# Optimization experiments

Measured on AMD Instinct MI355X. Metric: run time of the kernel, lower is better.

## Reference

```python
import jax, jax.numpy as jnp
import numpy as np

B = 2097152
IND = 10
DIM = 32
L = 4
M = DIM // 2 + 1  # 17 rfft bins
EPS = 1e-5


def setup_inputs() -> dict:
    key = jax.random.key(0)
    ks = jax.random.split(key, 16)
    scale = 1.0 / (DIM * DIM)
    inp = {
        'x': jax.random.normal(ks[0], (B, IND), dtype=jnp.float32),
        # stem / head Linear weights stored as [in, out] (x @ W + b)
        'stem_w': jax.random.normal(ks[1], (IND, DIM), jnp.float32) * (1.0 / np.sqrt(IND)),
        'stem_b': jnp.zeros((DIM,), jnp.float32),
        # Fourier weights: torch.rand complex -> real & imag ~ U[0,1), scaled
        'fno_wr': scale * jax.random.uniform(ks[2], (L, M, M), jnp.float32),
        'fno_wi': scale * jax.random.uniform(ks[3], (L, M, M), jnp.float32),
        # ResidualBlock params, stacked over layers
        'bn1_g': jnp.ones((L, DIM), jnp.float32),
        'bn1_b': jnp.zeros((L, DIM), jnp.float32),
        'lin1_w': jax.random.normal(ks[4], (L, DIM, DIM), jnp.float32) * (1.0 / np.sqrt(DIM)),
        'lin1_b': jnp.zeros((L, DIM), jnp.float32),
        'bn2_g': jnp.ones((L, DIM), jnp.float32),
        'bn2_b': jnp.zeros((L, DIM), jnp.float32),
        'lin2_w': jax.random.normal(ks[5], (L, DIM, DIM), jnp.float32) * (1.0 / np.sqrt(DIM)),
        'lin2_b': jnp.zeros((L, DIM), jnp.float32),
        'head_w': jax.random.normal(ks[6], (DIM, IND), jnp.float32) * (1.0 / np.sqrt(DIM)),
        'head_b': jnp.zeros((IND,), jnp.float32),
    }
    return inp


def _bn(h, g, b):
    # BatchNorm1d in training mode: biased batch stats over the batch dim
    mu = jnp.mean(h, axis=0)
    var = jnp.mean(jnp.square(h - mu), axis=0)
    return (h - mu) * jax.lax.rsqrt(var + EPS) * g + b


def reference(x, stem_w, stem_b, fno_wr, fno_wi, bn1_g, bn1_b, lin1_w, lin1_b,
              bn2_g, bn2_b, lin2_w, lin2_b, head_w, head_b):
    h = x @ stem_w + stem_b  # [B, DIM]
    n_layers = fno_wr.shape[0]
    for i in range(n_layers):
        # FourierBlock: rfft -> complex channel mix -> irfft (bias=False)
        w = fno_wr[i] + 1j * fno_wi[i]  # [M, M] complex
        hf = jnp.fft.rfft(h, axis=-1)  # [B, M] complex
        x1 = jnp.fft.irfft(hf @ w, n=DIM, axis=-1)  # [B, DIM]
        # ResidualBlock: BN -> SiLU -> Linear -> BN -> SiLU -> Linear, + identity skip
        r = jax.nn.silu(_bn(h, bn1_g[i], bn1_b[i])) @ lin1_w[i] + lin1_b[i]
        r = jax.nn.silu(_bn(r, bn2_g[i], bn2_b[i])) @ lin2_w[i] + lin2_b[i]
        x2 = r + h
        h = jax.nn.silu(x1 + x2)
    return h @ head_w + head_b  # [B, IND]
```

## Files before the change

### kernel.cpp

```cpp
#include <hip/hip_runtime.h>
#include <math.h>

#define BATCH   2097152
#define NTILES  (BATCH / 16)
#define GRID    2048
#define BLOCK   256
#define WAVES   (GRID * (BLOCK / 64))
#define NREP    16
#define NSETS   8

typedef __attribute__((ext_vector_type(8))) short short8;
typedef __attribute__((ext_vector_type(4))) float f32x4;
typedef unsigned short ushort_t;

__device__ __forceinline__ int chan_of(int s) { return (s >> 1) + ((s & 1) << 4); }

__device__ __forceinline__ float silu_f(float x) {
    return x * __builtin_amdgcn_rcpf(1.0f + __expf(-x));
}
__device__ __forceinline__ unsigned cvt_pk_bf16(float lo, float hi) {
    unsigned r;
    asm("v_cvt_pk_bf16_f32 %0, %1, %2" : "=v"(r) : "v"(lo), "v"(hi));
    return r;
}
__device__ __forceinline__ unsigned short f2bf(float f) {
    union { float f; unsigned u; } v; v.f = f;
    unsigned r = v.u + 0x7fffu + ((v.u >> 16) & 1u);
    return (unsigned short)(r >> 16);
}
__device__ __forceinline__ float bf2f(unsigned short b) {
    union { unsigned u; float f; } v; v.u = ((unsigned)b) << 16;
    return v.f;
}
__device__ __forceinline__ short8 pack8(const float* f) {
    union { short8 s; unsigned u[4]; } r;
    #pragma unroll
    for (int i = 0; i < 4; ++i) r.u[i] = cvt_pk_bf16(f[2 * i], f[2 * i + 1]);
    return r.s;
}
__device__ __forceinline__ f32x4 mfma16(short8 a, short8 b, f32x4 c) {
    return __builtin_amdgcn_mfma_f32_16x16x32_bf16(a, b, c, 0, 0, 0);
}
__device__ __forceinline__ short8 wfrag(const float* W, int ldN, int K, int lane, int half, int N) {
    short8 r;
    const int n = (lane & 15) + 16 * half;
    const int k0 = (lane >> 4) * 8;
    #pragma unroll
    for (int j = 0; j < 8; ++j) {
        const int ck = chan_of(k0 + j);
        const float v = (ck < K && n < N) ? W[ck * ldN + n] : 0.f;
        ((unsigned short*)&r)[j] = f2bf(v);
    }
    return r;
}
__device__ __forceinline__ void bn_coef(const double* sIn, const float* g, const float* b,
                                        int c, float* A, float* C) {
    double s = 0, q = 0;
    #pragma unroll
    for (int r = 0; r < NREP; ++r) { s += sIn[r * 64 + c]; q += sIn[r * 64 + 32 + c]; }
    const double inv = 1.0 / (double)BATCH;
    const double mu = s * inv, var = q * inv - mu * mu;
    const float a = (float)(1.0 / sqrt(var + 1e-5)) * g[c];
    *A = a; *C = b[c] - (float)mu * a;
}
__device__ __forceinline__ void stats_reduce_c(float sS0, float sQ0, float sS1, float sQ1,
                                               float (*sRed)[64], double* sOut, int tid) {
    const int lane = tid & 63, wid = tid >> 6;
    sS0 += __shfl_down(sS0, 32); sS0 += __shfl_down(sS0, 16);
    sQ0 += __shfl_down(sQ0, 32); sQ0 += __shfl_down(sQ0, 16);
    sS1 += __shfl_down(sS1, 32); sS1 += __shfl_down(sS1, 16);
    sQ1 += __shfl_down(sQ1, 32); sQ1 += __shfl_down(sQ1, 16);
    if (lane < 16) {
        sRed[wid][lane] = sS0; sRed[wid][16 + lane] = sS1;
        sRed[wid][32 + lane] = sQ0; sRed[wid][48 + lane] = sQ1;
    }
    __syncthreads();
    if (tid < 64) {
        const float tot = sRed[0][tid] + sRed[1][tid] + sRed[2][tid] + sRed[3][tid];
        atomicAdd(sOut + tid, (double)tot);
    }
}
__device__ __forceinline__ void stats_reduce_r(float* sLo, float* sQLo, float* sHi, float* sQHi,
                                               float (*sRed)[64], double* sOut, int tid) {
    const int lane = tid & 63, wid = tid >> 6, q = lane >> 4;
    #pragma unroll
    for (int r = 0; r < 4; ++r) {
        #pragma unroll
        for (int off = 8; off; off >>= 1) {
            sLo[r]  += __shfl_down(sLo[r],  off);
            sQLo[r] += __shfl_down(sQLo[r], off);
            sHi[r]  += __shfl_down(sHi[r],  off);
            sQHi[r] += __shfl_down(sQHi[r], off);
        }
    }
    if ((lane & 15) == 0) {
        #pragma unroll
        for (int r = 0; r < 4; ++r) {
            sRed[wid][q * 4 + r]      = sLo[r];
            sRed[wid][16 + q * 4 + r] = sHi[r];
            sRed[wid][32 + q * 4 + r] = sQLo[r];
            sRed[wid][48 + q * 4 + r] = sQHi[r];
        }
    }
    __syncthreads();
    if (tid < 64) {
        const float tot = sRed[0][tid] + sRed[1][tid] + sRed[2][tid] + sRed[3][tid];
        atomicAdd(sOut + tid, (double)tot);
    }
}

__global__ void setup_f_kernel(const float* __restrict__ wr, const float* __restrict__ wi,
                               float* __restrict__ Fp)
{
    __shared__ double cs[32], sn[32];
    const int l = blockIdx.x, tid = threadIdx.x;
    if (tid < 32) {
        double a = (2.0 * 3.14159265358979323846 / 32.0) * (double)tid;
        cs[tid] = cos(a); sn[tid] = sin(a);
    }
    __syncthreads();
    const float* wrl = wr + l * 289;
    const float* wil = wi + l * 289;
    for (int p = tid; p < 1024; p += BLOCK) {
        const int d = p >> 5, j = p & 31;
        double acc = 0.0;
        for (int m = 0; m < 17; ++m) {
            double yr = 0.0, yi = 0.0;
            for (int k = 0; k < 17; ++k) {
                const double c = cs[(k * d) & 31], s = sn[(k * d) & 31];
                const double a = (double)wrl[k * 17 + m], b = (double)wil[k * 17 + m];
                yr += c * a + s * b;
                yi += c * b - s * a;
            }
            const double alpha = (m == 0 || m == 16) ? 1.0 : 2.0;
            acc += alpha * (cs[(j * m) & 31] * yr - sn[(j * m) & 31] * yi);
        }
        const double F = acc * (1.0 / 32.0);
        Fp[l * 1024 + d * 32 + j] = (float)(F + ((d == j) ? 1.0 : 0.0));
    }
}

__global__ __launch_bounds__(BLOCK) void stem_kernel(
    const float* __restrict__ x, const float* __restrict__ sw, const float* __restrict__ sb,
    ushort_t* __restrict__ h, double* __restrict__ sOut)
{
    __shared__ float sRed[4][64];
    const int tid = threadIdx.x, lane = tid & 63, wid = tid >> 6;
    const int m = lane & 15, q = lane >> 4;
    const short8 B0 = wfrag(sw, 32, 10, lane, 0, 32);
    const short8 B1 = wfrag(sw, 32, 10, lane, 1, 32);
    float sblo[4], sbhi[4];
    #pragma unroll
    for (int r = 0; r < 4; ++r) { sblo[r] = sb[q * 4 + r]; sbhi[r] = sb[16 + q * 4 + r]; }
    float sLo[4] = {0,0,0,0}, sQLo[4] = {0,0,0,0}, sHi[4] = {0,0,0,0}, sQHi[4] = {0,0,0,0};
    for (int t = blockIdx.x * (BLOCK / 64) + wid; t < NTILES; t += WAVES) {
        const size_t rb = (size_t)t * 16;
        float c4[4];
        #pragma unroll
        for (int i2 = 0; i2 < 2; ++i2) {
            const int k = q * 4 + 2 * i2;
            if (k + 1 < 10) {
                const float2 v = *(const float2*)(x + (rb + m) * 10 + k);
                c4[2 * i2] = v.x; c4[2 * i2 + 1] = v.y;
            } else { c4[2 * i2] = 0.f; c4[2 * i2 + 1] = 0.f; }
        }
        float xv[8];
        #pragma unroll
        for (int j = 0; j < 8; ++j) xv[j] = (j & 1) ? 0.f : c4[j >> 1];
        const short8 xa = pack8(xv);
        f32x4 a0 = {sblo[0], sblo[1], sblo[2], sblo[3]};
        f32x4 a1 = {sbhi[0], sbhi[1], sbhi[2], sbhi[3]};
        a0 = mfma16(B0, xa, a0);
        a1 = mfma16(B1, xa, a1);
        #pragma unroll
        for (int r = 0; r < 4; ++r) {
            sLo[r] += a0[r]; sQLo[r] += a0[r] * a0[r];
            sHi[r] += a1[r]; sQHi[r] += a1[r] * a1[r];
            const unsigned w = cvt_pk_bf16(a0[r], a1[r]);
            *(unsigned*)(h + (rb + m) * 32 + (size_t)(q * 4 + r) * 2) = w;
        }
    }
    stats_reduce_r(sLo, sQLo, sHi, sQHi, sRed, sOut + (size_t)(blockIdx.x & (NREP - 1)) * 64, tid);
}

__global__ __launch_bounds__(BLOCK) void p1_kernel(
    const ushort_t* __restrict__ h_in, const double* __restrict__ sIn, double* __restrict__ sOut,
    const float* __restrict__ g1, const float* __restrict__ b1,
    const float* __restrict__ w1, const float* __restrict__ lb1)
{
    __shared__ float cA[32], cC[32];
    __shared__ float sRed[4][64];
    const int tid = threadIdx.x, lane = tid & 63, wid = tid >> 6;
    if (tid < 32) bn_coef(sIn, g1, b1, tid, &cA[tid], &cC[tid]);
    __syncthreads();
    const int m = lane & 15, q = lane >> 4;
    float a1k[8], c1k[8];
    #pragma unroll
    for (int j = 0; j < 8; ++j) {
        const int c = chan_of(q * 8 + j);
        a1k[j] = cA[c]; c1k[j] = cC[c];
    }
    const short8 W10 = wfrag(w1, 32, 32, lane, 0, 32);
    const short8 W11 = wfrag(w1, 32, 32, lane, 1, 32);
    const float lbc0 = lb1[m], lbc1 = lb1[m + 16];
    float sS0 = 0, sQ0 = 0, sS1 = 0, sQ1 = 0;
    for (int t = blockIdx.x * (BLOCK / 64) + wid; t < NTILES; t += WAVES) {
        const size_t rb = (size_t)t * 16;
        const short8 ha = *(const short8*)(h_in + (rb + m) * 32 + q * 8);
        float tf[8];
        #pragma unroll
        for (int j = 0; j < 8; ++j)
            tf[j] = silu_f(a1k[j] * bf2f(((const unsigned short*)&ha)[j]) + c1k[j]);
        const short8 ta = pack8(tf);
        f32x4 r0 = {lbc0, lbc0, lbc0, lbc0}, r1 = {lbc1, lbc1, lbc1, lbc1};
        r0 = mfma16(ta, W10, r0);
        r1 = mfma16(ta, W11, r1);
        #pragma unroll
        for (int r = 0; r < 4; ++r) {
            sS0 += r0[r]; sQ0 += r0[r] * r0[r];
            sS1 += r1[r]; sQ1 += r1[r] * r1[r];
        }
    }
    stats_reduce_c(sS0, sQ0, sS1, sQ1, sRed, sOut + (size_t)(blockIdx.x & (NREP - 1)) * 64, tid);
}

template<bool LAST>
__global__ __launch_bounds__(BLOCK) void p2_kernel(
    const ushort_t* __restrict__ h_in, ushort_t* __restrict__ h_out, float* __restrict__ out,
    const double* __restrict__ sIn1, const double* __restrict__ sIn2, double* __restrict__ sOut,
    const float* __restrict__ g1, const float* __restrict__ b1,
    const float* __restrict__ w1, const float* __restrict__ lb1,
    const float* __restrict__ g2, const float* __restrict__ b2,
    const float* __restrict__ w2, const float* __restrict__ lb2,
    const float* __restrict__ Fp, const float* __restrict__ hw, const float* __restrict__ hb)
{
    __shared__ float cA1[32], cC1[32], cA2[32], cD2[32];
    __shared__ float sRed[4][64];
    const int tid = threadIdx.x, lane = tid & 63, wid = tid >> 6;
    if (tid < 32) {
        bn_coef(sIn1, g1, b1, tid, &cA1[tid], &cC1[tid]);
    } else if (tid < 64) {
        const int c = tid - 32;
        float A, C;
        bn_coef(sIn2, g2, b2, c, &A, &C);
        cA2[c] = A; cD2[c] = C + A * lb1[c];
    }
    __syncthreads();
    const int m = lane & 15, q = lane >> 4;
    float a1k[8], c1k[8];
    #pragma unroll
    for (int j = 0; j < 8; ++j) {
        const int c = chan_of(q * 8 + j);
        a1k[j] = cA1[c]; c1k[j] = cC1[c];
    }
    float a2lo[4], d2lo[4], a2hi[4], d2hi[4], blo[4], bhi[4], hbl[4];
    #pragma unroll
    for (int r = 0; r < 4; ++r) {
        const int c = q * 4 + r;
        a2lo[r] = cA2[c];      d2lo[r] = cD2[c];
        a2hi[r] = cA2[c + 16]; d2hi[r] = cD2[c + 16];
        blo[r] = lb2[c];       bhi[r] = lb2[c + 16];
        hbl[r] = (LAST && c < 10) ? hb[c] : 0.f;
    }
    const short8 W10 = wfrag(w1, 32, 32, lane, 0, 32);
    const short8 W11 = wfrag(w1, 32, 32, lane, 1, 32);
    const short8 W20 = wfrag(w2, 32, 32, lane, 0, 32);
    const short8 W21 = wfrag(w2, 32, 32, lane, 1, 32);
    const short8 F0  = wfrag(Fp, 32, 32, lane, 0, 32);
    const short8 F1  = wfrag(Fp, 32, 32, lane, 1, 32);
    short8 HW = {};
    if (LAST) HW = wfrag(hw, 10, 32, lane, 0, 10);
    float sLo[4] = {0,0,0,0}, sQLo[4] = {0,0,0,0}, sHi[4] = {0,0,0,0}, sQHi[4] = {0,0,0,0};

    for (int t = blockIdx.x * (BLOCK / 64) + wid; t < NTILES; t += WAVES) {
        const size_t rb = (size_t)t * 16;
        const short8 ha = *(const short8*)(h_in + (rb + m) * 32 + q * 8);
        float tf[8];
        #pragma unroll
        for (int j = 0; j < 8; ++j)
            tf[j] = silu_f(a1k[j] * bf2f(((const unsigned short*)&ha)[j]) + c1k[j]);
        const short8 ta = pack8(tf);
        const f32x4 z = {0.f, 0.f, 0.f, 0.f};
        f32x4 r0 = mfma16(W10, ta, z);
        f32x4 r1 = mfma16(W11, ta, z);
        float ulo[4], uhi[4];
        #pragma unroll
        for (int r = 0; r < 4; ++r) {
            ulo[r] = silu_f(a2lo[r] * r0[r] + d2lo[r]);
            uhi[r] = silu_f(a2hi[r] * r1[r] + d2hi[r]);
        }
        union { short8 s; unsigned u[4]; } uau;
        #pragma unroll
        for (int i = 0; i < 4; ++i) uau.u[i] = cvt_pk_bf16(ulo[i], uhi[i]);
        const short8 ua = uau.s;
        f32x4 c0 = {blo[0], blo[1], blo[2], blo[3]};
        f32x4 c1 = {bhi[0], bhi[1], bhi[2], bhi[3]};
        c0 = mfma16(F0, ha, c0);  c1 = mfma16(F1, ha, c1);
        c0 = mfma16(W20, ua, c0); c1 = mfma16(W21, ua, c1);
        float hnlo[4], hnhi[4];
        #pragma unroll
        for (int r = 0; r < 4; ++r) { hnlo[r] = silu_f(c0[r]); hnhi[r] = silu_f(c1[r]); }
        if (!LAST) {
            #pragma unroll
            for (int r = 0; r < 4; ++r) {
                sLo[r] += hnlo[r]; sQLo[r] += hnlo[r] * hnlo[r];
                sHi[r] += hnhi[r]; sQHi[r] += hnhi[r] * hnhi[r];
                const unsigned w = cvt_pk_bf16(hnlo[r], hnhi[r]);
                *(unsigned*)(h_out + (rb + m) * 32 + (size_t)(q * 4 + r) * 2) = w;
            }
        } else {
            union { short8 s; unsigned u[4]; } hnu;
            #pragma unroll
            for (int i = 0; i < 4; ++i) hnu.u[i] = cvt_pk_bf16(hnlo[i], hnhi[i]);
            f32x4 oc = {hbl[0], hbl[1], hbl[2], hbl[3]};
            oc = mfma16(HW, hnu.s, oc);
            #pragma unroll
            for (int r = 0; r < 4; ++r)
                if (q * 4 + r < 10) out[(rb + m) * 10 + q * 4 + r] = oc[r];
        }
    }
    if (!LAST)
        stats_reduce_r(sLo, sQLo, sHi, sQHi, sRed, sOut + (size_t)(blockIdx.x & (NREP - 1)) * 64, tid);
}

extern "C" void kernel_launch(void* const* d_in, const int* in_sizes, int n_in,
                              void* d_out, int out_size, void* d_ws, size_t ws_size,
                              hipStream_t stream)
{
    const float* x      = (const float*)d_in[0];
    const float* stem_w = (const float*)d_in[1];
    const float* stem_b = (const float*)d_in[2];
    const float* fno_wr = (const float*)d_in[3];
    const float* fno_wi = (const float*)d_in[4];
    const float* bn1_g  = (const float*)d_in[5];
    const float* bn1_b  = (const float*)d_in[6];
    const float* lin1_w = (const float*)d_in[7];
    const float* lin1_b = (const float*)d_in[8];
    const float* bn2_g  = (const float*)d_in[9];
    const float* bn2_b  = (const float*)d_in[10];
    const float* lin2_w = (const float*)d_in[11];
    const float* lin2_b = (const float*)d_in[12];
    const float* head_w = (const float*)d_in[13];
    const float* head_b = (const float*)d_in[14];

    ushort_t* h  = (ushort_t*)d_ws;
    float*    Fp = (float*)((char*)d_ws + (size_t)BATCH * 32 * sizeof(ushort_t));
    double*   st = (double*)((char*)d_ws + (size_t)BATCH * 32 * sizeof(ushort_t) + 16384);

    hipMemsetAsync(st, 0, (size_t)NSETS * NREP * 64 * sizeof(double), stream);
    setup_f_kernel<<<4, BLOCK, 0, stream>>>(fno_wr, fno_wi, Fp);
    stem_kernel<<<GRID, BLOCK, 0, stream>>>(x, stem_w, stem_b, h, st);

    for (int l = 0; l < 4; ++l) {
        double* sH = st + (size_t)(2 * l) * NREP * 64;
        double* sR = st + (size_t)(2 * l + 1) * NREP * 64;
        p1_kernel<<<GRID, BLOCK, 0, stream>>>(
            h, sH, sR,
            bn1_g + l * 32, bn1_b + l * 32, lin1_w + l * 1024, lin1_b + l * 32);
        if (l < 3) {
            double* sN = st + (size_t)(2 * l + 2) * NREP * 64;
            p2_kernel<false><<<GRID, BLOCK, 0, stream>>>(
                h, h, nullptr, sH, sR, sN,
                bn1_g + l * 32, bn1_b + l * 32, lin1_w + l * 1024, lin1_b + l * 32,
                bn2_g + l * 32, bn2_b + l * 32, lin2_w + l * 1024, lin2_b + l * 32,
                Fp + l * 1024, nullptr, nullptr);
        } else {
            p2_kernel<true><<<GRID, BLOCK, 0, stream>>>(
                h, nullptr, (float*)d_out, sH, sR, st,
                bn1_g + l * 32, bn1_b + l * 32, lin1_w + l * 1024, lin1_b + l * 32,
                bn2_g + l * 32, bn2_b + l * 32, lin2_w + l * 1024, lin2_b + l * 32,
                Fp + l * 1024, head_w, head_b);
        }
    }
}
```

Before: 634.1 us.

## Cache BN1+SiLU activations from p1 for reuse in p2; vectorize stores

When the workspace is large enough, p1 writes the bf16 BN1+SiLU activation tile to a second buffer and p2 loads it instead of recomputing the normalization and SiLU. The h stores in stem and p2 are merged into single 16-byte short8 writes, and the head output uses float2 stores. This trades per-element exp/rcp work in p2 for an extra 128 MB write in p1 and read in p2 per layer. On a kernel that is already memory-bound, that extra traffic may cost more than the compute it saves.

```diff
diff --git a/kernel.cpp b/kernel.cpp
--- a/kernel.cpp
+++ b/kernel.cpp
@@ -172,19 +172,22 @@
         f32x4 a1 = {sbhi[0], sbhi[1], sbhi[2], sbhi[3]};
         a0 = mfma16(B0, xa, a0);
         a1 = mfma16(B1, xa, a1);
+        union { short8 s; unsigned u[4]; } hw_;
         #pragma unroll
         for (int r = 0; r < 4; ++r) {
             sLo[r] += a0[r]; sQLo[r] += a0[r] * a0[r];
             sHi[r] += a1[r]; sQHi[r] += a1[r] * a1[r];
-            const unsigned w = cvt_pk_bf16(a0[r], a1[r]);
-            *(unsigned*)(h + (rb + m) * 32 + (size_t)(q * 4 + r) * 2) = w;
-        }
+            hw_.u[r] = cvt_pk_bf16(a0[r], a1[r]);
+        }
+        *(short8*)(h + (rb + m) * 32 + q * 8) = hw_.s;
     }
     stats_reduce_r(sLo, sQLo, sHi, sQHi, sRed, sOut + (size_t)(blockIdx.x & (NREP - 1)) * 64, tid);
 }
 
+template<bool STORE_T>
 __global__ __launch_bounds__(BLOCK) void p1_kernel(
-    const ushort_t* __restrict__ h_in, const double* __restrict__ sIn, double* __restrict__ sOut,
+    const ushort_t* __restrict__ h_in, ushort_t* __restrict__ t_out,
+    const double* __restrict__ sIn, double* __restrict__ sOut,
     const float* __restrict__ g1, const float* __restrict__ b1,
     const float* __restrict__ w1, const float* __restrict__ lb1)
 {
@@ -212,6 +215,8 @@
         for (int j = 0; j < 8; ++j)
             tf[j] = silu_f(a1k[j] * bf2f(((const unsigned short*)&ha)[j]) + c1k[j]);
         const short8 ta = pack8(tf);
+        if (STORE_T)
+            *(short8*)(t_out + (rb + m) * 32 + q * 8) = ta;
         f32x4 r0 = {lbc0, lbc0, lbc0, lbc0}, r1 = {lbc1, lbc1, lbc1, lbc1};
         r0 = mfma16(ta, W10, r0);
         r1 = mfma16(ta, W11, r1);
@@ -224,9 +229,10 @@
     stats_reduce_c(sS0, sQ0, sS1, sQ1, sRed, sOut + (size_t)(blockIdx.x & (NREP - 1)) * 64, tid);
 }
 
-template<bool LAST>
+template<bool LAST, bool TLOAD>
 __global__ __launch_bounds__(BLOCK) void p2_kernel(
-    const ushort_t* __restrict__ h_in, ushort_t* __restrict__ h_out, float* __restrict__ out,
+    const ushort_t* __restrict__ h_in, const ushort_t* __restrict__ t_in,
+    ushort_t* __restrict__ h_out, float* __restrict__ out,
     const double* __restrict__ sIn1, const double* __restrict__ sIn2, double* __restrict__ sOut,
     const float* __restrict__ g1, const float* __restrict__ b1,
     const float* __restrict__ w1, const float* __restrict__ lb1,
@@ -248,10 +254,12 @@
     __syncthreads();
     const int m = lane & 15, q = lane >> 4;
     float a1k[8], c1k[8];
-    #pragma unroll
-    for (int j = 0; j < 8; ++j) {
-        const int c = chan_of(q * 8 + j);
-        a1k[j] = cA1[c]; c1k[j] = cC1[c];
+    if (!TLOAD) {
+        #pragma unroll
+        for (int j = 0; j < 8; ++j) {
+            const int c = chan_of(q * 8 + j);
+            a1k[j] = cA1[c]; c1k[j] = cC1[c];
+        }
     }
     float a2lo[4], d2lo[4], a2hi[4], d2hi[4], blo[4], bhi[4], hbl[4];
     #pragma unroll
@@ -275,11 +283,16 @@
     for (int t = blockIdx.x * (BLOCK / 64) + wid; t < NTILES; t += WAVES) {
         const size_t rb = (size_t)t * 16;
         const short8 ha = *(const short8*)(h_in + (rb + m) * 32 + q * 8);
-        float tf[8];
-        #pragma unroll
-        for (int j = 0; j < 8; ++j)
-            tf[j] = silu_f(a1k[j] * bf2f(((const unsigned short*)&ha)[j]) + c1k[j]);
-        const short8 ta = pack8(tf);
+        short8 ta;
+        if (TLOAD) {
+            ta = *(const short8*)(t_in + (rb + m) * 32 + q * 8);
+        } else {
+            float tf[8];
+            #pragma unroll
+            for (int j = 0; j < 8; ++j)
+                tf[j] = silu_f(a1k[j] * bf2f(((const unsigned short*)&ha)[j]) + c1k[j]);
+            ta = pack8(tf);
+        }
         const f32x4 z = {0.f, 0.f, 0.f, 0.f};
         f32x4 r0 = mfma16(W10, ta, z);
         f32x4 r1 = mfma16(W11, ta, z);
@@ -300,23 +313,28 @@
         float hnlo[4], hnhi[4];
         #pragma unroll
         for (int r = 0; r < 4; ++r) { hnlo[r] = silu_f(c0[r]); hnhi[r] = silu_f(c1[r]); }
+        union { short8 s; unsigned u[4]; } hnu;
+        #pragma unroll
+        for (int r = 0; r < 4; ++r) hnu.u[r] = cvt_pk_bf16(hnlo[r], hnhi[r]);
         if (!LAST) {
             #pragma unroll
             for (int r = 0; r < 4; ++r) {
                 sLo[r] += hnlo[r]; sQLo[r] += hnlo[r] * hnlo[r];
                 sHi[r] += hnhi[r]; sQHi[r] += hnhi[r] * hnhi[r];
-                const unsigned w = cvt_pk_bf16(hnlo[r], hnhi[r]);
-                *(unsigned*)(h_out + (rb + m) * 32 + (size_t)(q * 4 + r) * 2) = w;
             }
+            *(short8*)(h_out + (rb + m) * 32 + q * 8) = hnu.s;
         } else {
-            union { short8 s; unsigned u[4]; } hnu;
-            #pragma unroll
-            for (int i = 0; i < 4; ++i) hnu.u[i] = cvt_pk_bf16(hnlo[i], hnhi[i]);
             f32x4 oc = {hbl[0], hbl[1], hbl[2], hbl[3]};
             oc = mfma16(HW, hnu.s, oc);
-            #pragma unroll
-            for (int r = 0; r < 4; ++r)
-                if (q * 4 + r < 10) out[(rb + m) * 10 + q * 4 + r] = oc[r];
+            float* op = out + (rb + m) * 10 + q * 4;
+            if (q < 2) {
+                float2 v0; v0.x = oc[0]; v0.y = oc[1];
+                float2 v1; v1.x = oc[2]; v1.y = oc[3];
+                *(float2*)op = v0; *(float2*)(op + 2) = v1;
+            } else if (q == 2) {
+                float2 v0; v0.x = oc[0]; v0.y = oc[1];
+                *(float2*)op = v0;
+            }
         }
     }
     if (!LAST)
@@ -343,9 +361,15 @@
     const float* head_w = (const float*)d_in[13];
     const float* head_b = (const float*)d_in[14];
 
+    const size_t HBYTES = (size_t)BATCH * 32 * sizeof(ushort_t);
+    const size_t TAIL   = 16384 + (size_t)NSETS * NREP * 64 * sizeof(double);
+    const bool   big    = ws_size >= 2 * HBYTES + TAIL;
+
     ushort_t* h  = (ushort_t*)d_ws;
-    float*    Fp = (float*)((char*)d_ws + (size_t)BATCH * 32 * sizeof(ushort_t));
-    double*   st = (double*)((char*)d_ws + (size_t)BATCH * 32 * sizeof(ushort_t) + 16384);
+    ushort_t* tw = big ? (ushort_t*)((char*)d_ws + HBYTES) : nullptr;
+    char*     tp = (char*)d_ws + (big ? 2 * HBYTES : HBYTES);
+    float*    Fp = (float*)tp;
+    double*   st = (double*)(tp + 16384);
 
     hipMemsetAsync(st, 0, (size_t)NSETS * NREP * 64 * sizeof(double), stream);
     setup_f_kernel<<<4, BLOCK, 0, stream>>>(fno_wr, fno_wi, Fp);
@@ -354,22 +378,39 @@
     for (int l = 0; l < 4; ++l) {
         double* sH = st + (size_t)(2 * l) * NREP * 64;
         double* sR = st + (size_t)(2 * l + 1) * NREP * 64;
-        p1_kernel<<<GRID, BLOCK, 0, stream>>>(
-            h, sH, sR,
-            bn1_g + l * 32, bn1_b + l * 32, lin1_w + l * 1024, lin1_b + l * 32);
-        if (l < 3) {
-            double* sN = st + (size_t)(2 * l + 2) * NREP * 64;
-            p2_kernel<false><<<GRID, BLOCK, 0, stream>>>(
-                h, h, nullptr, sH, sR, sN,
-                bn1_g + l * 32, bn1_b + l * 32, lin1_w + l * 1024, lin1_b + l * 32,
-                bn2_g + l * 32, bn2_b + l * 32, lin2_w + l * 1024, lin2_b + l * 32,
-                Fp + l * 1024, nullptr, nullptr);
+        double* sN = (l < 3) ? st + (size_t)(2 * l + 2) * NREP * 64 : st;
+        if (big) {
+            p1_kernel<true><<<GRID, BLOCK, 0, stream>>>(
+                h, tw, sH, sR,
+                bn1_g + l * 32, bn1_b + l * 32, lin1_w + l * 1024, lin1_b + l * 32);
+            if (l < 3)
+                p2_kernel<false, true><<<GRID, BLOCK, 0, stream>>>(
+                    h, tw, h, nullptr, sH, sR, sN,
+                    bn1_g + l * 32, bn1_b + l * 32, lin1_w + l * 1024, lin1_b + l * 32,
+                    bn2_g + l * 32, bn2_b + l * 32, lin2_w + l * 1024, lin2_b + l * 32,
+                    Fp + l * 1024, nullptr, nullptr);
+            else
+                p2_kernel<true, true><<<GRID, BLOCK, 0, stream>>>(
+                    h, tw, nullptr, (float*)d_out, sH, sR, st,
+                    bn1_g + l * 32, bn1_b + l * 32, lin1_w + l * 1024, lin1_b + l * 32,
+                    bn2_g + l * 32, bn2_b + l * 32, lin2_w + l * 1024, lin2_b + l * 32,
+                    Fp + l * 1024, head_w, head_b);
         } else {
-            p2_kernel<true><<<GRID, BLOCK, 0, stream>>>(
-                h, nullptr, (float*)d_out, sH, sR, st,
-                bn1_g + l * 32, bn1_b + l * 32, lin1_w + l * 1024, lin1_b + l * 32,
-                bn2_g + l * 32, bn2_b + l * 32, lin2_w + l * 1024, lin2_b + l * 32,
-                Fp + l * 1024, head_w, head_b);
-        }
-    }
-}
+            p1_kernel<false><<<GRID, BLOCK, 0, stream>>>(
+                h, nullptr, sH, sR,
+                bn1_g + l * 32, bn1_b + l * 32, lin1_w + l * 1024, lin1_b + l * 32);
+            if (l < 3)
+                p2_kernel<false, false><<<GRID, BLOCK, 0, stream>>>(
+                    h, nullptr, h, nullptr, sH, sR, sN,
+                    bn1_g + l * 32, bn1_b + l * 32, lin1_w + l * 1024, lin1_b + l * 32,
+                    bn2_g + l * 32, bn2_b + l * 32, lin2_w + l * 1024, lin2_b + l * 32,
+                    Fp + l * 1024, nullptr, nullptr);
+            else
+                p2_kernel<true, false><<<GRID, BLOCK, 0, stream>>>(
+                    h, nullptr, nullptr, (float*)d_out, sH, sR, st,
+                    bn1_g + l * 32, bn1_b + l * 32, lin1_w + l * 1024, lin1_b + l * 32,
+                    bn2_g + l * 32, bn2_b + l * 32, lin2_w + l * 1024, lin2_b + l * 32,
+                    Fp + l * 1024, head_w, head_b);
+        }
+    }
+}
```

Measured after the change: 726.6 us. 1.15x slower.

## Software-pipeline tile loads and vectorize bf16 and output stores

Applied to the files above, without the earlier changes.

The grid-stride loops in p1 and p2 now process two tiles per iteration and issue the loads for the next pair before computing the current pair, so global load latency overlaps with MFMA and SiLU work. The bf16 hidden-state writes in the stem and p2 kernels become one 16-byte store per lane instead of four 4-byte stores. The final-layer output writes use float2 stores. The loop now assumes NTILES divides evenly by 2*WAVES and keeps more live registers, which may reduce occupancy.

```diff
diff --git a/kernel.cpp b/kernel.cpp
--- a/kernel.cpp
+++ b/kernel.cpp
@@ -6,6 +6,7 @@
 #define GRID    2048
 #define BLOCK   256
 #define WAVES   (GRID * (BLOCK / 64))
+#define NIT2    (NTILES / WAVES / 2)
 #define NREP    16
 #define NSETS   8
 
@@ -172,13 +173,14 @@
         f32x4 a1 = {sbhi[0], sbhi[1], sbhi[2], sbhi[3]};
         a0 = mfma16(B0, xa, a0);
         a1 = mfma16(B1, xa, a1);
+        union { short8 s; unsigned u[4]; } hw_;
         #pragma unroll
         for (int r = 0; r < 4; ++r) {
             sLo[r] += a0[r]; sQLo[r] += a0[r] * a0[r];
             sHi[r] += a1[r]; sQHi[r] += a1[r] * a1[r];
-            const unsigned w = cvt_pk_bf16(a0[r], a1[r]);
-            *(unsigned*)(h + (rb + m) * 32 + (size_t)(q * 4 + r) * 2) = w;
-        }
+            hw_.u[r] = cvt_pk_bf16(a0[r], a1[r]);
+        }
+        *(short8*)(h + (rb + m) * 32 + q * 8) = hw_.s;
     }
     stats_reduce_r(sLo, sQLo, sHi, sQHi, sRed, sOut + (size_t)(blockIdx.x & (NREP - 1)) * 64, tid);
 }
@@ -204,9 +206,8 @@
     const short8 W11 = wfrag(w1, 32, 32, lane, 1, 32);
     const float lbc0 = lb1[m], lbc1 = lb1[m + 16];
     float sS0 = 0, sQ0 = 0, sS1 = 0, sQ1 = 0;
-    for (int t = blockIdx.x * (BLOCK / 64) + wid; t < NTILES; t += WAVES) {
-        const size_t rb = (size_t)t * 16;
-        const short8 ha = *(const short8*)(h_in + (rb + m) * 32 + q * 8);
+
+    auto process = [&](const short8 ha) {
         float tf[8];
         #pragma unroll
         for (int j = 0; j < 8; ++j)
@@ -220,6 +221,23 @@
             sS0 += r0[r]; sQ0 += r0[r] * r0[r];
             sS1 += r1[r]; sQ1 += r1[r] * r1[r];
         }
+    };
+
+    const size_t RSTEP = (size_t)WAVES * 16;
+    const int qo = q * 8;
+    size_t rowA = (size_t)(blockIdx.x * (BLOCK / 64) + wid) * 16 + m;
+    size_t rowB = rowA + RSTEP;
+    short8 haA = *(const short8*)(h_in + rowA * 32 + qo);
+    short8 haB = *(const short8*)(h_in + rowB * 32 + qo);
+    for (int i = 0; i < NIT2; ++i) {
+        const bool more = (i + 1 < NIT2);
+        const size_t rA2 = more ? rowA + 2 * RSTEP : rowA;
+        const size_t rB2 = more ? rowB + 2 * RSTEP : rowB;
+        const short8 pfA = *(const short8*)(h_in + rA2 * 32 + qo);
+        const short8 pfB = *(const short8*)(h_in + rB2 * 32 + qo);
+        process(haA);
+        process(haB);
+        haA = pfA; haB = pfB; rowA = rA2; rowB = rB2;
     }
     stats_reduce_c(sS0, sQ0, sS1, sQ1, sRed, sOut + (size_t)(blockIdx.x & (NREP - 1)) * 64, tid);
 }
@@ -271,10 +289,9 @@
     short8 HW = {};
     if (LAST) HW = wfrag(hw, 10, 32, lane, 0, 10);
     float sLo[4] = {0,0,0,0}, sQLo[4] = {0,0,0,0}, sHi[4] = {0,0,0,0}, sQHi[4] = {0,0,0,0};
-
-    for (int t = blockIdx.x * (BLOCK / 64) + wid; t < NTILES; t += WAVES) {
-        const size_t rb = (size_t)t * 16;
-        const short8 ha = *(const short8*)(h_in + (rb + m) * 32 + q * 8);
+    const int qo = q * 8;
+
+    auto process = [&](const short8 ha, const size_t row) {
         float tf[8];
         #pragma unroll
         for (int j = 0; j < 8; ++j)
@@ -292,32 +309,52 @@
         union { short8 s; unsigned u[4]; } uau;
         #pragma unroll
         for (int i = 0; i < 4; ++i) uau.u[i] = cvt_pk_bf16(ulo[i], uhi[i]);
-        const short8 ua = uau.s;
         f32x4 c0 = {blo[0], blo[1], blo[2], blo[3]};
         f32x4 c1 = {bhi[0], bhi[1], bhi[2], bhi[3]};
         c0 = mfma16(F0, ha, c0);  c1 = mfma16(F1, ha, c1);
-        c0 = mfma16(W20, ua, c0); c1 = mfma16(W21, ua, c1);
+        c0 = mfma16(W20, uau.s, c0); c1 = mfma16(W21, uau.s, c1);
         float hnlo[4], hnhi[4];
         #pragma unroll
         for (int r = 0; r < 4; ++r) { hnlo[r] = silu_f(c0[r]); hnhi[r] = silu_f(c1[r]); }
+        union { short8 s; unsigned u[4]; } hnu;
+        #pragma unroll
+        for (int r = 0; r < 4; ++r) hnu.u[r] = cvt_pk_bf16(hnlo[r], hnhi[r]);
         if (!LAST) {
             #pragma unroll
             for (int r = 0; r < 4; ++r) {
                 sLo[r] += hnlo[r]; sQLo[r] += hnlo[r] * hnlo[r];
                 sHi[r] += hnhi[r]; sQHi[r] += hnhi[r] * hnhi[r];
-                const unsigned w = cvt_pk_bf16(hnlo[r], hnhi[r]);
-                *(unsigned*)(h_out + (rb + m) * 32 + (size_t)(q * 4 + r) * 2) = w;
             }
+            *(short8*)(h_out + row * 32 + qo) = hnu.s;
         } else {
-            union { short8 s; unsigned u[4]; } hnu;
-            #pragma unroll
-            for (int i = 0; i < 4; ++i) hnu.u[i] = cvt_pk_bf16(hnlo[i], hnhi[i]);
             f32x4 oc = {hbl[0], hbl[1], hbl[2], hbl[3]};
             oc = mfma16(HW, hnu.s, oc);
-            #pragma unroll
-            for (int r = 0; r < 4; ++r)
-                if (q * 4 + r < 10) out[(rb + m) * 10 + q * 4 + r] = oc[r];
-        }
+            float* op = out + row * 10 + q * 4;
+            if (q < 2) {
+                float2 v0; v0.x = oc[0]; v0.y = oc[1];
+                float2 v1; v1.x = oc[2]; v1.y = oc[3];
+                *(float2*)op = v0; *(float2*)(op + 2) = v1;
+            } else if (q == 2) {
+                float2 v0; v0.x = oc[0]; v0.y = oc[1];
+                *(float2*)op = v0;
+            }
+        }
+    };
+
+    const size_t RSTEP = (size_t)WAVES * 16;
+    size_t rowA = (size_t)(blockIdx.x * (BLOCK / 64) + wid) * 16 + m;
+    size_t rowB = rowA + RSTEP;
+    short8 haA = *(const short8*)(h_in + rowA * 32 + qo);
+    short8 haB = *(const short8*)(h_in + rowB * 32 + qo);
+    for (int i = 0; i < NIT2; ++i) {
+        const bool more = (i + 1 < NIT2);
+        const size_t rA2 = more ? rowA + 2 * RSTEP : rowA;
+        const size_t rB2 = more ? rowB + 2 * RSTEP : rowB;
+        const short8 pfA = *(const short8*)(h_in + rA2 * 32 + qo);
+        const short8 pfB = *(const short8*)(h_in + rB2 * 32 + qo);
+        process(haA, rowA);
+        process(haB, rowB);
+        haA = pfA; haB = pfB; rowA = rA2; rowB = rB2;
     }
     if (!LAST)
         stats_reduce_r(sLo, sQLo, sHi, sQHi, sRed, sOut + (size_t)(blockIdx.x & (NREP - 1)) * 64, tid);
```

After: 628.8 us. No clear change (-0.8%).

## Prefetch activation tiles into LDS with a 4-deep async pipeline and vectorize stores

Applied to the files above, without the earlier changes.

The p1 and p2 loops now use global_load_lds to prefetch the bf16 activation tiles four iterations ahead into a per-wave LDS ring. Hand-placed vmcnt waits track the outstanding loads, and the per-wave loop is fully unrolled over a fixed tile count. The stem and p2 kernels also write h as one 16-byte store instead of four 4-byte stores, and the final output uses float2 stores. The aim is to hide global memory latency and cut store transactions. In exchange the vmcnt counts are hardcoded to a specific store and load mix and must stay exact, which makes the code fragile.

```diff
diff --git a/kernel.cpp b/kernel.cpp
--- a/kernel.cpp
+++ b/kernel.cpp
@@ -6,12 +6,16 @@
 #define GRID    2048
 #define BLOCK   256
 #define WAVES   (GRID * (BLOCK / 64))
+#define NTPW    (NTILES / WAVES)
+#define DEPTH   4
 #define NREP    16
 #define NSETS   8
 
 typedef __attribute__((ext_vector_type(8))) short short8;
 typedef __attribute__((ext_vector_type(4))) float f32x4;
 typedef unsigned short ushort_t;
+
+#define WAITVM(N) asm volatile("s_waitcnt vmcnt(" #N ")" ::: "memory")
 
 __device__ __forceinline__ int chan_of(int s) { return (s >> 1) + ((s & 1) << 4); }
 
@@ -40,6 +44,11 @@
 }
 __device__ __forceinline__ f32x4 mfma16(short8 a, short8 b, f32x4 c) {
     return __builtin_amdgcn_mfma_f32_16x16x32_bf16(a, b, c, 0, 0, 0);
+}
+__device__ __forceinline__ void stage1k(const ushort_t* g, ushort_t* l) {
+    __builtin_amdgcn_global_load_lds(
+        (const __attribute__((address_space(1))) unsigned int*)g,
+        (__attribute__((address_space(3))) unsigned int*)l, 16, 0, 0);
 }
 __device__ __forceinline__ short8 wfrag(const float* W, int ldN, int K, int lane, int half, int N) {
     short8 r;
@@ -172,13 +181,14 @@
         f32x4 a1 = {sbhi[0], sbhi[1], sbhi[2], sbhi[3]};
         a0 = mfma16(B0, xa, a0);
         a1 = mfma16(B1, xa, a1);
+        union { short8 s; unsigned u[4]; } hw_;
         #pragma unroll
         for (int r = 0; r < 4; ++r) {
             sLo[r] += a0[r]; sQLo[r] += a0[r] * a0[r];
             sHi[r] += a1[r]; sQHi[r] += a1[r] * a1[r];
-            const unsigned w = cvt_pk_bf16(a0[r], a1[r]);
-            *(unsigned*)(h + (rb + m) * 32 + (size_t)(q * 4 + r) * 2) = w;
-        }
+            hw_.u[r] = cvt_pk_bf16(a0[r], a1[r]);
+        }
+        *(short8*)(h + (rb + m) * 32 + q * 8) = hw_.s;
     }
     stats_reduce_r(sLo, sQLo, sHi, sQHi, sRed, sOut + (size_t)(blockIdx.x & (NREP - 1)) * 64, tid);
 }
@@ -190,6 +200,7 @@
 {
     __shared__ float cA[32], cC[32];
     __shared__ float sRed[4][64];
+    __shared__ ushort_t stage[4][DEPTH][512] __attribute__((aligned(16)));
     const int tid = threadIdx.x, lane = tid & 63, wid = tid >> 6;
     if (tid < 32) bn_coef(sIn, g1, b1, tid, &cA[tid], &cC[tid]);
     __syncthreads();
@@ -204,9 +215,26 @@
     const short8 W11 = wfrag(w1, 32, 32, lane, 1, 32);
     const float lbc0 = lb1[m], lbc1 = lb1[m + 16];
     float sS0 = 0, sQ0 = 0, sS1 = 0, sQ1 = 0;
-    for (int t = blockIdx.x * (BLOCK / 64) + wid; t < NTILES; t += WAVES) {
-        const size_t rb = (size_t)t * 16;
-        const short8 ha = *(const short8*)(h_in + (rb + m) * 32 + q * 8);
+
+    const int gwid = blockIdx.x * (BLOCK / 64) + wid;
+    const size_t GSTRIDE = (size_t)WAVES * 512;
+    const ushort_t* gsrc = h_in + ((size_t)gwid * 16 + m) * 32 + q * 8;
+    ushort_t (*stg)[512] = stage[wid];
+    #pragma unroll
+    for (int d = 0; d < DEPTH; ++d) stage1k(gsrc + (size_t)d * GSTRIDE, &stg[d][0]);
+
+    #pragma unroll
+    for (int i = 0; i < NTPW; ++i) {
+        if (i <= 12)      WAITVM(3);
+        else if (i == 13) WAITVM(2);
+        else if (i == 14) WAITVM(1);
+        else              WAITVM(0);
+        __builtin_amdgcn_sched_barrier(0);
+        const short8 ha = *(const short8*)(&stg[i & (DEPTH - 1)][lane * 8]);
+        asm volatile("s_waitcnt lgkmcnt(0)" ::: "memory");
+        __builtin_amdgcn_sched_barrier(0);
+        if (i + DEPTH < NTPW)
+            stage1k(gsrc + (size_t)(i + DEPTH) * GSTRIDE, &stg[i & (DEPTH - 1)][0]);
         float tf[8];
         #pragma unroll
         for (int j = 0; j < 8; ++j)
@@ -236,6 +264,7 @@
 {
     __shared__ float cA1[32], cC1[32], cA2[32], cD2[32];
     __shared__ float sRed[4][64];
+    __shared__ ushort_t stage[4][DEPTH][512] __attribute__((aligned(16)));
     const int tid = threadIdx.x, lane = tid & 63, wid = tid >> 6;
     if (tid < 32) {
         bn_coef(sIn1, g1, b1, tid, &cA1[tid], &cC1[tid]);
@@ -272,9 +301,42 @@
     if (LAST) HW = wfrag(hw, 10, 32, lane, 0, 10);
     float sLo[4] = {0,0,0,0}, sQLo[4] = {0,0,0,0}, sHi[4] = {0,0,0,0}, sQHi[4] = {0,0,0,0};
 
-    for (int t = blockIdx.x * (BLOCK / 64) + wid; t < NTILES; t += WAVES) {
-        const size_t rb = (size_t)t * 16;
-        const short8 ha = *(const short8*)(h_in + (rb + m) * 32 + q * 8);
+    const int gwid = blockIdx.x * (BLOCK / 64) + wid;
+    const size_t GSTRIDE = (size_t)WAVES * 512;
+    const ushort_t* gsrc = h_in + ((size_t)gwid * 16 + m) * 32 + q * 8;
+    ushort_t (*stg)[512] = stage[wid];
+    #pragma unroll
+    for (int d = 0; d < DEPTH; ++d) stage1k(gsrc + (size_t)d * GSTRIDE, &stg[d][0]);
+
+    #pragma unroll
+    for (int i = 0; i < NTPW; ++i) {
+        if (LAST) {
+            if      (i == 0)  WAITVM(3);
+            else if (i == 1)  WAITVM(6);
+            else if (i == 2)  WAITVM(9);
+            else if (i == 3)  WAITVM(12);
+            else if (i <= 12) WAITVM(15);
+            else if (i == 13) WAITVM(14);
+            else if (i == 14) WAITVM(13);
+            else              WAITVM(12);
+        } else {
+            if      (i == 0)  WAITVM(3);
+            else if (i == 1)  WAITVM(4);
+            else if (i == 2)  WAITVM(5);
+            else if (i == 3)  WAITVM(6);
+            else if (i <= 12) WAITVM(7);
+            else if (i == 13) WAITVM(6);
+            else if (i == 14) WAITVM(5);
+            else              WAITVM(4);
+        }
+        __builtin_amdgcn_sched_barrier(0);
+        const short8 ha = *(const short8*)(&stg[i & (DEPTH - 1)][lane * 8]);
+        asm volatile("s_waitcnt lgkmcnt(0)" ::: "memory");
+        __builtin_amdgcn_sched_barrier(0);
+        if (i + DEPTH < NTPW)
+            stage1k(gsrc + (size_t)(i + DEPTH) * GSTRIDE, &stg[i & (DEPTH - 1)][0]);
+
+        const size_t row = (size_t)(gwid + i * WAVES) * 16 + m;
         float tf[8];
         #pragma unroll
         for (int j = 0; j < 8; ++j)
@@ -291,32 +353,36 @@
         }
         union { short8 s; unsigned u[4]; } uau;
         #pragma unroll
-        for (int i = 0; i < 4; ++i) uau.u[i] = cvt_pk_bf16(ulo[i], uhi[i]);
-        const short8 ua = uau.s;
+        for (int k = 0; k < 4; ++k) uau.u[k] = cvt_pk_bf16(ulo[k], uhi[k]);
         f32x4 c0 = {blo[0], blo[1], blo[2], blo[3]};
         f32x4 c1 = {bhi[0], bhi[1], bhi[2], bhi[3]};
         c0 = mfma16(F0, ha, c0);  c1 = mfma16(F1, ha, c1);
-        c0 = mfma16(W20, ua, c0); c1 = mfma16(W21, ua, c1);
+        c0 = mfma16(W20, uau.s, c0); c1 = mfma16(W21, uau.s, c1);
         float hnlo[4], hnhi[4];
         #pragma unroll
         for (int r = 0; r < 4; ++r) { hnlo[r] = silu_f(c0[r]); hnhi[r] = silu_f(c1[r]); }
+        union { short8 s; unsigned u[4]; } hnu;
+        #pragma unroll
+        for (int r = 0; r < 4; ++r) hnu.u[r] = cvt_pk_bf16(hnlo[r], hnhi[r]);
         if (!LAST) {
             #pragma unroll
             for (int r = 0; r < 4; ++r) {
                 sLo[r] += hnlo[r]; sQLo[r] += hnlo[r] * hnlo[r];
                 sHi[r] += hnhi[r]; sQHi[r] += hnhi[r] * hnhi[r];
-                const unsigned w = cvt_pk_bf16(hnlo[r], hnhi[r]);
-                *(unsigned*)(h_out + (rb + m) * 32 + (size_t)(q * 4 + r) * 2) = w;
             }
+            *(short8*)(h_out + row * 32 + q * 8) = hnu.s;
         } else {
-            union { short8 s; unsigned u[4]; } hnu;
-            #pragma unroll
-            for (int i = 0; i < 4; ++i) hnu.u[i] = cvt_pk_bf16(hnlo[i], hnhi[i]);
             f32x4 oc = {hbl[0], hbl[1], hbl[2], hbl[3]};
             oc = mfma16(HW, hnu.s, oc);
-            #pragma unroll
-            for (int r = 0; r < 4; ++r)
-                if (q * 4 + r < 10) out[(rb + m) * 10 + q * 4 + r] = oc[r];
+            float* op = out + row * 10 + q * 4;
+            if (q < 2) {
+                float2 v0; v0.x = oc[0]; v0.y = oc[1];
+                float2 v1; v1.x = oc[2]; v1.y = oc[3];
+                *(float2*)op = v0; *(float2*)(op + 2) = v1;
+            } else if (q == 2) {
+                float2 v0; v0.x = oc[0]; v0.y = oc[1];
+                *(float2*)op = v0;
+            }
         }
     }
     if (!LAST)
```

Result: slower. 648.7 us (+2.3%).
